# Optimization experiments

Measured on AMD Instinct MI355X. Metric: run time of the kernel, lower is better.

Reference implementation:

```python
import jax, jax.numpy as jnp
import numpy as np

B, F, L, D = 256, 4, 64, 768
HID = (F + F) * 200  # 1600
NEG = -1e10


def setup_inputs() -> dict:
    key = jax.random.key(0)
    ks = jax.random.split(key, 8)
    left = jax.random.normal(ks[0], (B, F, L, D), dtype=jnp.float32)
    right = jax.random.normal(ks[1], (B, F, L, D), dtype=jnp.float32)
    # emulate ragged padding: last quarter of tokens are zero (masked out)
    left = left.at[:, :, 3 * L // 4 :, :].set(0.0)
    right = right.at[:, :, 3 * L // 4 :, :].set(0.0)
    femb_l = jax.random.normal(ks[2], (F, D), dtype=jnp.float32)
    femb_r = jax.random.normal(ks[3], (F, D), dtype=jnp.float32)
    empty_attr = jax.random.normal(ks[4], (D,), dtype=jnp.float32) * 0.05
    in_dim = 2 * F * D
    W1 = jax.random.normal(ks[5], (HID, in_dim), dtype=jnp.float32) * (1.0 / np.sqrt(in_dim))
    b1 = jnp.zeros((HID,), dtype=jnp.float32)
    W2 = jax.random.normal(ks[6], (2, HID), dtype=jnp.float32) * (1.0 / np.sqrt(HID))
    b2 = jnp.full((2,), -np.log((1 - 0.01) / 0.01), dtype=jnp.float32)
    return {"left": left, "right": right, "femb_l": femb_l, "femb_r": femb_r,
            "empty_attr": empty_attr, "W1": W1, "b1": b1, "W2": W2, "b2": b2}


def _attribute_matching(v, femb, empty_attr):
    # v: [B, F, L, D], femb: [F, D]
    tok_mask = (v != 0).sum(axis=-1) > 0          # [B, F, L]
    attr_mask = tok_mask.any(axis=-1)              # [B, F]
    logits = jnp.einsum('bfld,fd->bfl', v, femb)   # per-field attention scores
    logits = logits + jnp.where(tok_mask, 0.0, NEG)
    w = jax.nn.softmax(logits, axis=2)             # masked softmax over tokens
    summary = jnp.einsum('bfl,bfld->bfd', w, v)    # attention pooling
    return jnp.where(attr_mask[..., None], summary, empty_attr)  # [B, F, D]


def reference(left, right, femb_l, femb_r, empty_attr, W1, b1, W2, b2):
    l_rep = _attribute_matching(left, femb_l, empty_attr)
    r_rep = _attribute_matching(right, femb_r, empty_attr)
    concat = jnp.concatenate([l_rep, r_rep], axis=1).reshape(left.shape[0], -1)
    h = jax.nn.relu(concat @ W1.T + b1)
    return h @ W2.T + b2  # [B, 2]
```

## Files before the change

### kernel.cpp

```cpp
#include <hip/hip_runtime.h>

typedef __attribute__((ext_vector_type(8))) short short8;
typedef __attribute__((ext_vector_type(4))) short short4_t;
typedef __attribute__((ext_vector_type(4))) float f32x4;

#define NEGBIG -1e10f

__device__ __forceinline__ unsigned short f2bf(float x) {
  unsigned int u = __float_as_uint(x);
  u += 0x7FFFu + ((u >> 16) & 1u);
  return (unsigned short)(u >> 16);
}
__device__ __forceinline__ unsigned pack2(float a, float b) {
  unsigned ua = __float_as_uint(a), ub = __float_as_uint(b);
  ua += 0x7FFFu + ((ua >> 16) & 1u);
  ub += 0x7FFFu + ((ub >> 16) & 1u);
  return (ua >> 16) | (ub & 0xFFFF0000u);
}
__device__ __forceinline__ float lo_bf(unsigned p) { return __uint_as_float(p << 16); }
__device__ __forceinline__ float hi_bf(unsigned p) { return __uint_as_float(p & 0xFFFF0000u); }

__device__ __forceinline__ float4 mul4(float4 a, float s) {
  float4 r; r.x = a.x*s; r.y = a.y*s; r.z = a.z*s; r.w = a.w*s; return r;
}
__device__ __forceinline__ float4 add4(float4 a, float4 b) {
  float4 r; r.x = a.x+b.x; r.y = a.y+b.y; r.z = a.z+b.z; r.w = a.w+b.w; return r;
}

__global__ __launch_bounds__(256) void pool_partial(
    const float* __restrict__ left, const float* __restrict__ right,
    const float* __restrict__ femb_l, const float* __restrict__ femb_r,
    float* __restrict__ partials,
    float4* __restrict__ meta)
{
  int bid   = blockIdx.x;
  int panel = bid >> 1;
  int half  = bid & 1;
  int side  = panel >> 10;
  int rem   = panel & 1023;
  int f     = rem & 3;
  const float* v    = (side ? right : left) + (size_t)rem * 64 * 768 + (size_t)half * 32 * 768;
  const float* femb = (side ? femb_r : femb_l) + f * 768;

  int tid = threadIdx.x, wave = tid >> 6, lane = tid & 63;

  const float4* fp = (const float4*)femb;
  float4 f0 = fp[lane], f1 = fp[lane + 64], f2 = fp[lane + 128];

  const float4* vp = (const float4*)(v + (size_t)wave * 8 * 768);

  float d[8];
  unsigned pk0[8], pk1[8], pk2[8], pk3[8], pk4[8], pk5[8];
  unsigned nzmask = 0;

  #pragma unroll
  for (int t = 0; t < 8; ++t) {
    float4 x0 = vp[t * 192 + lane];
    float4 x1 = vp[t * 192 + 64 + lane];
    float4 x2 = vp[t * 192 + 128 + lane];
    d[t] = x0.x*f0.x + x0.y*f0.y + x0.z*f0.z + x0.w*f0.w
         + x1.x*f1.x + x1.y*f1.y + x1.z*f1.z + x1.w*f1.w
         + x2.x*f2.x + x2.y*f2.y + x2.z*f2.z + x2.w*f2.w;
    unsigned nzb = __float_as_uint(x0.x) | __float_as_uint(x0.y)
                 | __float_as_uint(x0.z) | __float_as_uint(x0.w)
                 | __float_as_uint(x1.x) | __float_as_uint(x1.y)
                 | __float_as_uint(x1.z) | __float_as_uint(x1.w)
                 | __float_as_uint(x2.x) | __float_as_uint(x2.y)
                 | __float_as_uint(x2.z) | __float_as_uint(x2.w);
    nzmask |= (nzb != 0u) ? (1u << t) : 0u;
    pk0[t] = pack2(x0.x, x0.y); pk1[t] = pack2(x0.z, x0.w);
    pk2[t] = pack2(x1.x, x1.y); pk3[t] = pack2(x1.z, x1.w);
    pk4[t] = pack2(x2.x, x2.y); pk5[t] = pack2(x2.z, x2.w);
  }

  #pragma unroll
  for (int sh = 32; sh > 0; sh >>= 1) {
    d[0] += __shfl_xor(d[0], sh);
    d[1] += __shfl_xor(d[1], sh);
    d[2] += __shfl_xor(d[2], sh);
    d[3] += __shfl_xor(d[3], sh);
    d[4] += __shfl_xor(d[4], sh);
    d[5] += __shfl_xor(d[5], sh);
    d[6] += __shfl_xor(d[6], sh);
    d[7] += __shfl_xor(d[7], sh);
    nzmask |= __shfl_xor(nzmask, sh);
  }

  float l[8], e[8];
  #pragma unroll
  for (int t = 0; t < 8; ++t)
    l[t] = d[t] + (((nzmask >> t) & 1u) ? 0.f : NEGBIG);
  float m01 = fmaxf(l[0], l[1]), m23 = fmaxf(l[2], l[3]);
  float m45 = fmaxf(l[4], l[5]), m67 = fmaxf(l[6], l[7]);
  float m_w = fmaxf(fmaxf(m01, m23), fmaxf(m45, m67));
  #pragma unroll
  for (int t = 0; t < 8; ++t) e[t] = __expf(l[t] - m_w);
  float s_w = ((e[0]+e[1]) + (e[2]+e[3])) + ((e[4]+e[5]) + (e[6]+e[7]));

  __shared__ float m_lds[4], s_lds[4];
  __shared__ int   nz_lds[4];
  __shared__ float acc_lds[4 * 768];

  if (lane == 0) { m_lds[wave] = m_w; s_lds[wave] = s_w; nz_lds[wave] = (nzmask != 0u); }

  float4 A0 = {0,0,0,0}, A1 = {0,0,0,0}, A2 = {0,0,0,0};
  #pragma unroll
  for (int t = 0; t < 8; ++t) {
    float c = e[t];
    A0.x += c * lo_bf(pk0[t]); A0.y += c * hi_bf(pk0[t]);
    A0.z += c * lo_bf(pk1[t]); A0.w += c * hi_bf(pk1[t]);
    A1.x += c * lo_bf(pk2[t]); A1.y += c * hi_bf(pk2[t]);
    A1.z += c * lo_bf(pk3[t]); A1.w += c * hi_bf(pk3[t]);
    A2.x += c * lo_bf(pk4[t]); A2.y += c * hi_bf(pk4[t]);
    A2.z += c * lo_bf(pk5[t]); A2.w += c * hi_bf(pk5[t]);
  }

  __syncthreads();
  float M = fmaxf(fmaxf(m_lds[0], m_lds[1]), fmaxf(m_lds[2], m_lds[3]));
  float S = s_lds[0] * __expf(m_lds[0] - M) + s_lds[1] * __expf(m_lds[1] - M)
          + s_lds[2] * __expf(m_lds[2] - M) + s_lds[3] * __expf(m_lds[3] - M);
  float scale = __expf(m_w - M);

  float4* al = (float4*)acc_lds;
  al[wave * 192 +       lane] = mul4(A0, scale);
  al[wave * 192 +  64 + lane] = mul4(A1, scale);
  al[wave * 192 + 128 + lane] = mul4(A2, scale);
  __syncthreads();

  if (tid < 192) {
    float4 A = add4(add4(al[tid], al[192 + tid]),
                    add4(al[384 + tid], al[576 + tid]));
    ((float4*)(partials + (size_t)bid * 768))[tid] = A;
  }
  if (tid == 192) {
    int has = nz_lds[0] | nz_lds[1] | nz_lds[2] | nz_lds[3];
    float4 mt; mt.x = M; mt.y = S; mt.z = has ? 1.f : 0.f; mt.w = 0.f;
    meta[bid] = mt;
  }
}

__global__ __launch_bounds__(192) void pool_merge(
    const float* __restrict__ partials, const float4* __restrict__ meta,
    const float* __restrict__ empty_attr,
    unsigned short* __restrict__ concat)
{
  int panel = blockIdx.x;
  int tid = threadIdx.x;
  int side = panel >> 10;
  int rem  = panel & 1023;
  int f    = rem & 3;
  int b    = rem >> 2;

  float4 mt0 = meta[panel * 2], mt1 = meta[panel * 2 + 1];
  float M = fmaxf(mt0.x, mt1.x);
  float sc0 = __expf(mt0.x - M), sc1 = __expf(mt1.x - M);
  float S = mt0.y * sc0 + mt1.y * sc1;
  int has = (mt0.z != 0.f) | (mt1.z != 0.f);

  float4 A0 = ((const float4*)(partials + (size_t)(panel * 2) * 768))[tid];
  float4 A1 = ((const float4*)(partials + (size_t)(panel * 2 + 1) * 768))[tid];
  float4 r;
  if (has) {
    float inv = 1.f / S;
    r = add4(mul4(A0, sc0 * inv), mul4(A1, sc1 * inv));
  } else {
    r = ((const float4*)empty_attr)[tid];
  }
  ushort4 o;
  o.x = f2bf(r.x); o.y = f2bf(r.y); o.z = f2bf(r.z); o.w = f2bf(r.w);
  size_t base = ((size_t)b * 8 + side * 4 + f) * 192;
  ((ushort4*)concat)[base + tid] = o;
}

__global__ __launch_bounds__(256) void gemm1_kernel(
    const unsigned short* __restrict__ A,
    const float* __restrict__ W1,
    float* __restrict__ Hpart)
{
  const int K = 6144, N = 1600, KC = 768;
  int colb = blockIdx.x;
  int kc   = blockIdx.y;
  int col0 = colb * 16;
  int tid = threadIdx.x, wave = tid >> 6, lane = tid & 63;

  __shared__ short wlds[96 * 16 * 8];

  const float* wsrc = W1 + (size_t)col0 * K + kc * KC;
  #pragma unroll
  for (int i = 0; i < 12; ++i) {
    int flat4 = tid + 256 * i;
    int col = flat4 / 192;
    int k   = (flat4 % 192) * 4;
    float4 w = *(const float4*)(wsrc + (size_t)col * K + k);
    short4_t o;
    o[0] = (short)f2bf(w.x); o[1] = (short)f2bf(w.y);
    o[2] = (short)f2bf(w.z); o[3] = (short)f2bf(w.w);
    *(short4_t*)(wlds + (k >> 3) * 128 + col * 8 + (k & 7)) = o;
  }
  __syncthreads();

  int lr = lane & 15;
  const short* a0 = (const short*)A + (size_t)(wave * 64 + lr) * K + kc * KC + (lane >> 4) * 8;
  const short* bptr = wlds + (lane >> 4) * 128 + lr * 8;

  f32x4 acc0 = {}, acc1 = {}, acc2 = {}, acc3 = {};

  #pragma unroll 4
  for (int ks = 0; ks < 24; ++ks) {
    short8 bf  = *(const short8*)(bptr + ks * 512);
    short8 af0 = *(const short8*)(a0 + ks * 32);
    short8 af1 = *(const short8*)(a0 + ks * 32 + 16 * K);
    short8 af2 = *(const short8*)(a0 + ks * 32 + 32 * K);
    short8 af3 = *(const short8*)(a0 + ks * 32 + 48 * K);
    acc0 = __builtin_amdgcn_mfma_f32_16x16x32_bf16(af0, bf, acc0, 0, 0, 0);
    acc1 = __builtin_amdgcn_mfma_f32_16x16x32_bf16(af1, bf, acc1, 0, 0, 0);
    acc2 = __builtin_amdgcn_mfma_f32_16x16x32_bf16(af2, bf, acc2, 0, 0, 0);
    acc3 = __builtin_amdgcn_mfma_f32_16x16x32_bf16(af3, bf, acc3, 0, 0, 0);
  }

  int ccol = lane & 15;
  int crow = (lane >> 4) * 4;
  float* hp = Hpart + (size_t)kc * 256 * N + (size_t)col0 + ccol;
  f32x4 accs[4] = {acc0, acc1, acc2, acc3};
  #pragma unroll
  for (int i = 0; i < 4; ++i) {
    int r = wave * 64 + i * 16 + crow;
    #pragma unroll
    for (int q = 0; q < 4; ++q)
      hp[(size_t)(r + q) * N] = accs[i][q];
  }
}

__global__ __launch_bounds__(256) void epilogue_kernel(
    const float* __restrict__ Hpart, const float* __restrict__ b1,
    const float* __restrict__ W2, const float* __restrict__ b2,
    float* __restrict__ out)
{
  const int N = 1600;
  int b = blockIdx.x, tid = threadIdx.x;
  int wave = tid >> 6, lane = tid & 63;
  float s0 = 0.f, s1 = 0.f;
  for (int c = tid; c < N; c += 256) {
    float acc = 0.f;
    #pragma unroll
    for (int kc = 0; kc < 8; ++kc)
      acc += Hpart[((size_t)kc * 256 + b) * N + c];
    float h = fmaxf(acc + b1[c], 0.f);
    s0 += h * W2[c];
    s1 += h * W2[N + c];
  }
  #pragma unroll
  for (int s = 32; s > 0; s >>= 1) {
    s0 += __shfl_xor(s0, s);
    s1 += __shfl_xor(s1, s);
  }
  __shared__ float r0[4], r1[4];
  if (lane == 0) { r0[wave] = s0; r1[wave] = s1; }
  __syncthreads();
  if (tid == 0) {
    out[b * 2 + 0] = r0[0] + r0[1] + r0[2] + r0[3] + b2[0];
    out[b * 2 + 1] = r1[0] + r1[1] + r1[2] + r1[3] + b2[1];
  }
}

extern "C" void kernel_launch(void* const* d_in, const int* in_sizes, int n_in,
                              void* d_out, int out_size, void* d_ws, size_t ws_size,
                              hipStream_t stream) {
  const float* left       = (const float*)d_in[0];
  const float* right      = (const float*)d_in[1];
  const float* femb_l     = (const float*)d_in[2];
  const float* femb_r     = (const float*)d_in[3];
  const float* empty_attr = (const float*)d_in[4];
  const float* W1         = (const float*)d_in[5];
  const float* b1         = (const float*)d_in[6];
  const float* W2         = (const float*)d_in[7];
  const float* b2         = (const float*)d_in[8];
  float* out = (float*)d_out;

  char* ws = (char*)d_ws;
  unsigned short* concat = (unsigned short*)ws;
  float*          Hpart  = (float*)(ws + 3145728);
  float*  partials = Hpart;
  float4* meta     = (float4*)(ws + 3145728 + 12582912);

  hipLaunchKernelGGL(pool_partial, dim3(4096), dim3(256), 0, stream,
                     left, right, femb_l, femb_r, partials, meta);
  hipLaunchKernelGGL(pool_merge, dim3(2048), dim3(192), 0, stream,
                     partials, meta, empty_attr, concat);
  hipLaunchKernelGGL(gemm1_kernel, dim3(100, 8), dim3(256), 0, stream,
                     concat, W1, Hpart);
  hipLaunchKernelGGL(epilogue_kernel, dim3(256), dim3(256), 0, stream,
                     Hpart, b1, W2, b2, out);
}
```

Before: 139.6 us.

## Split pooling into quarter-panel blocks and store partials in bf16

Each pooling block now handles 16 tokens instead of 32, doubling the grid to 8192 blocks with fewer live registers per thread and an occupancy hint in launch bounds. Partial sums are written as bf16 instead of fp32, and the merge kernel combines four partials with log-sum-exp rescaling. This aims to improve memory latency hiding on the bandwidth-bound input read and to cut intermediate traffic. In exchange it adds one more rounding step on the partial sums, and the merge kernel does more work.

```diff
diff --git a/kernel.cpp b/kernel.cpp
--- a/kernel.cpp
+++ b/kernel.cpp
@@ -19,6 +19,7 @@
 }
 __device__ __forceinline__ float lo_bf(unsigned p) { return __uint_as_float(p << 16); }
 __device__ __forceinline__ float hi_bf(unsigned p) { return __uint_as_float(p & 0xFFFF0000u); }
+__device__ __forceinline__ float bfu(unsigned short h) { return __uint_as_float(((unsigned)h) << 16); }
 
 __device__ __forceinline__ float4 mul4(float4 a, float s) {
   float4 r; r.x = a.x*s; r.y = a.y*s; r.z = a.z*s; r.w = a.w*s; return r;
@@ -27,19 +28,19 @@
   float4 r; r.x = a.x+b.x; r.y = a.y+b.y; r.z = a.z+b.z; r.w = a.w+b.w; return r;
 }
 
-__global__ __launch_bounds__(256) void pool_partial(
+__global__ __launch_bounds__(256, 4) void pool_partial(
     const float* __restrict__ left, const float* __restrict__ right,
     const float* __restrict__ femb_l, const float* __restrict__ femb_r,
-    float* __restrict__ partials,
+    unsigned short* __restrict__ partials,
     float4* __restrict__ meta)
 {
-  int bid   = blockIdx.x;
-  int panel = bid >> 1;
-  int half  = bid & 1;
-  int side  = panel >> 10;
-  int rem   = panel & 1023;
-  int f     = rem & 3;
-  const float* v    = (side ? right : left) + (size_t)rem * 64 * 768 + (size_t)half * 32 * 768;
+  int bid     = blockIdx.x;
+  int panel   = bid >> 2;
+  int quarter = bid & 3;
+  int side    = panel >> 10;
+  int rem     = panel & 1023;
+  int f       = rem & 3;
+  const float* v    = (side ? right : left) + (size_t)rem * 64 * 768 + (size_t)quarter * 16 * 768;
   const float* femb = (side ? femb_r : femb_l) + f * 768;
 
   int tid = threadIdx.x, wave = tid >> 6, lane = tid & 63;
@@ -47,30 +48,47 @@
   const float4* fp = (const float4*)femb;
   float4 f0 = fp[lane], f1 = fp[lane + 64], f2 = fp[lane + 128];
 
-  const float4* vp = (const float4*)(v + (size_t)wave * 8 * 768);
-
-  float d[8];
-  unsigned pk0[8], pk1[8], pk2[8], pk3[8], pk4[8], pk5[8];
+  const float4* vp = (const float4*)(v + (size_t)wave * 4 * 768);
+
+  float d[4];
+  unsigned pk[4][6];
   unsigned nzmask = 0;
 
   #pragma unroll
-  for (int t = 0; t < 8; ++t) {
-    float4 x0 = vp[t * 192 + lane];
-    float4 x1 = vp[t * 192 + 64 + lane];
-    float4 x2 = vp[t * 192 + 128 + lane];
-    d[t] = x0.x*f0.x + x0.y*f0.y + x0.z*f0.z + x0.w*f0.w
-         + x1.x*f1.x + x1.y*f1.y + x1.z*f1.z + x1.w*f1.w
-         + x2.x*f2.x + x2.y*f2.y + x2.z*f2.z + x2.w*f2.w;
-    unsigned nzb = __float_as_uint(x0.x) | __float_as_uint(x0.y)
-                 | __float_as_uint(x0.z) | __float_as_uint(x0.w)
-                 | __float_as_uint(x1.x) | __float_as_uint(x1.y)
-                 | __float_as_uint(x1.z) | __float_as_uint(x1.w)
-                 | __float_as_uint(x2.x) | __float_as_uint(x2.y)
-                 | __float_as_uint(x2.z) | __float_as_uint(x2.w);
-    nzmask |= (nzb != 0u) ? (1u << t) : 0u;
-    pk0[t] = pack2(x0.x, x0.y); pk1[t] = pack2(x0.z, x0.w);
-    pk2[t] = pack2(x1.x, x1.y); pk3[t] = pack2(x1.z, x1.w);
-    pk4[t] = pack2(x2.x, x2.y); pk5[t] = pack2(x2.z, x2.w);
+  for (int g = 0; g < 2; ++g) {
+    const float4* ta = vp + (g * 2 + 0) * 192 + lane;
+    const float4* tb = vp + (g * 2 + 1) * 192 + lane;
+    float4 xa0 = ta[0], xa1 = ta[64], xa2 = ta[128];
+    float4 xb0 = tb[0], xb1 = tb[64], xb2 = tb[128];
+
+    int t0 = g * 2, t1 = g * 2 + 1;
+    d[t0] = xa0.x*f0.x + xa0.y*f0.y + xa0.z*f0.z + xa0.w*f0.w
+          + xa1.x*f1.x + xa1.y*f1.y + xa1.z*f1.z + xa1.w*f1.w
+          + xa2.x*f2.x + xa2.y*f2.y + xa2.z*f2.z + xa2.w*f2.w;
+    unsigned nza = __float_as_uint(xa0.x) | __float_as_uint(xa0.y)
+                 | __float_as_uint(xa0.z) | __float_as_uint(xa0.w)
+                 | __float_as_uint(xa1.x) | __float_as_uint(xa1.y)
+                 | __float_as_uint(xa1.z) | __float_as_uint(xa1.w)
+                 | __float_as_uint(xa2.x) | __float_as_uint(xa2.y)
+                 | __float_as_uint(xa2.z) | __float_as_uint(xa2.w);
+    nzmask |= (nza != 0u) ? (1u << t0) : 0u;
+    pk[t0][0] = pack2(xa0.x, xa0.y); pk[t0][1] = pack2(xa0.z, xa0.w);
+    pk[t0][2] = pack2(xa1.x, xa1.y); pk[t0][3] = pack2(xa1.z, xa1.w);
+    pk[t0][4] = pack2(xa2.x, xa2.y); pk[t0][5] = pack2(xa2.z, xa2.w);
+
+    d[t1] = xb0.x*f0.x + xb0.y*f0.y + xb0.z*f0.z + xb0.w*f0.w
+          + xb1.x*f1.x + xb1.y*f1.y + xb1.z*f1.z + xb1.w*f1.w
+          + xb2.x*f2.x + xb2.y*f2.y + xb2.z*f2.z + xb2.w*f2.w;
+    unsigned nzb = __float_as_uint(xb0.x) | __float_as_uint(xb0.y)
+                 | __float_as_uint(xb0.z) | __float_as_uint(xb0.w)
+                 | __float_as_uint(xb1.x) | __float_as_uint(xb1.y)
+                 | __float_as_uint(xb1.z) | __float_as_uint(xb1.w)
+                 | __float_as_uint(xb2.x) | __float_as_uint(xb2.y)
+                 | __float_as_uint(xb2.z) | __float_as_uint(xb2.w);
+    nzmask |= (nzb != 0u) ? (1u << t1) : 0u;
+    pk[t1][0] = pack2(xb0.x, xb0.y); pk[t1][1] = pack2(xb0.z, xb0.w);
+    pk[t1][2] = pack2(xb1.x, xb1.y); pk[t1][3] = pack2(xb1.z, xb1.w);
+    pk[t1][4] = pack2(xb2.x, xb2.y); pk[t1][5] = pack2(xb2.z, xb2.w);
   }
 
   #pragma unroll
@@ -79,23 +97,17 @@
     d[1] += __shfl_xor(d[1], sh);
     d[2] += __shfl_xor(d[2], sh);
     d[3] += __shfl_xor(d[3], sh);
-    d[4] += __shfl_xor(d[4], sh);
-    d[5] += __shfl_xor(d[5], sh);
-    d[6] += __shfl_xor(d[6], sh);
-    d[7] += __shfl_xor(d[7], sh);
     nzmask |= __shfl_xor(nzmask, sh);
   }
 
-  float l[8], e[8];
-  #pragma unroll
-  for (int t = 0; t < 8; ++t)
+  float l[4], e[4];
+  #pragma unroll
+  for (int t = 0; t < 4; ++t)
     l[t] = d[t] + (((nzmask >> t) & 1u) ? 0.f : NEGBIG);
-  float m01 = fmaxf(l[0], l[1]), m23 = fmaxf(l[2], l[3]);
-  float m45 = fmaxf(l[4], l[5]), m67 = fmaxf(l[6], l[7]);
-  float m_w = fmaxf(fmaxf(m01, m23), fmaxf(m45, m67));
-  #pragma unroll
-  for (int t = 0; t < 8; ++t) e[t] = __expf(l[t] - m_w);
-  float s_w = ((e[0]+e[1]) + (e[2]+e[3])) + ((e[4]+e[5]) + (e[6]+e[7]));
+  float m_w = fmaxf(fmaxf(l[0], l[1]), fmaxf(l[2], l[3]));
+  #pragma unroll
+  for (int t = 0; t < 4; ++t) e[t] = __expf(l[t] - m_w);
+  float s_w = (e[0] + e[1]) + (e[2] + e[3]);
 
   __shared__ float m_lds[4], s_lds[4];
   __shared__ int   nz_lds[4];
@@ -105,14 +117,14 @@
 
   float4 A0 = {0,0,0,0}, A1 = {0,0,0,0}, A2 = {0,0,0,0};
   #pragma unroll
-  for (int t = 0; t < 8; ++t) {
+  for (int t = 0; t < 4; ++t) {
     float c = e[t];
-    A0.x += c * lo_bf(pk0[t]); A0.y += c * hi_bf(pk0[t]);
-    A0.z += c * lo_bf(pk1[t]); A0.w += c * hi_bf(pk1[t]);
-    A1.x += c * lo_bf(pk2[t]); A1.y += c * hi_bf(pk2[t]);
-    A1.z += c * lo_bf(pk3[t]); A1.w += c * hi_bf(pk3[t]);
-    A2.x += c * lo_bf(pk4[t]); A2.y += c * hi_bf(pk4[t]);
-    A2.z += c * lo_bf(pk5[t]); A2.w += c * hi_bf(pk5[t]);
+    A0.x += c * lo_bf(pk[t][0]); A0.y += c * hi_bf(pk[t][0]);
+    A0.z += c * lo_bf(pk[t][1]); A0.w += c * hi_bf(pk[t][1]);
+    A1.x += c * lo_bf(pk[t][2]); A1.y += c * hi_bf(pk[t][2]);
+    A1.z += c * lo_bf(pk[t][3]); A1.w += c * hi_bf(pk[t][3]);
+    A2.x += c * lo_bf(pk[t][4]); A2.y += c * hi_bf(pk[t][4]);
+    A2.z += c * lo_bf(pk[t][5]); A2.w += c * hi_bf(pk[t][5]);
   }
 
   __syncthreads();
@@ -130,7 +142,9 @@
   if (tid < 192) {
     float4 A = add4(add4(al[tid], al[192 + tid]),
                     add4(al[384 + tid], al[576 + tid]));
-    ((float4*)(partials + (size_t)bid * 768))[tid] = A;
+    ushort4 o;
+    o.x = f2bf(A.x); o.y = f2bf(A.y); o.z = f2bf(A.z); o.w = f2bf(A.w);
+    ((ushort4*)(partials + (size_t)bid * 768))[tid] = o;
   }
   if (tid == 192) {
     int has = nz_lds[0] | nz_lds[1] | nz_lds[2] | nz_lds[3];
@@ -140,7 +154,7 @@
 }
 
 __global__ __launch_bounds__(192) void pool_merge(
-    const float* __restrict__ partials, const float4* __restrict__ meta,
+    const unsigned short* __restrict__ partials, const float4* __restrict__ meta,
     const float* __restrict__ empty_attr,
     unsigned short* __restrict__ concat)
 {
@@ -151,18 +165,26 @@
   int f    = rem & 3;
   int b    = rem >> 2;
 
-  float4 mt0 = meta[panel * 2], mt1 = meta[panel * 2 + 1];
-  float M = fmaxf(mt0.x, mt1.x);
+  int p4 = panel * 4;
+  float4 mt0 = meta[p4], mt1 = meta[p4 + 1], mt2 = meta[p4 + 2], mt3 = meta[p4 + 3];
+  float M = fmaxf(fmaxf(mt0.x, mt1.x), fmaxf(mt2.x, mt3.x));
   float sc0 = __expf(mt0.x - M), sc1 = __expf(mt1.x - M);
-  float S = mt0.y * sc0 + mt1.y * sc1;
-  int has = (mt0.z != 0.f) | (mt1.z != 0.f);
-
-  float4 A0 = ((const float4*)(partials + (size_t)(panel * 2) * 768))[tid];
-  float4 A1 = ((const float4*)(partials + (size_t)(panel * 2 + 1) * 768))[tid];
+  float sc2 = __expf(mt2.x - M), sc3 = __expf(mt3.x - M);
+  float S = mt0.y * sc0 + mt1.y * sc1 + mt2.y * sc2 + mt3.y * sc3;
+  int has = (mt0.z + mt1.z + mt2.z + mt3.z) != 0.f;
+
+  ushort4 q0 = ((const ushort4*)(partials + (size_t)(p4 + 0) * 768))[tid];
+  ushort4 q1 = ((const ushort4*)(partials + (size_t)(p4 + 1) * 768))[tid];
+  ushort4 q2 = ((const ushort4*)(partials + (size_t)(p4 + 2) * 768))[tid];
+  ushort4 q3 = ((const ushort4*)(partials + (size_t)(p4 + 3) * 768))[tid];
+
   float4 r;
   if (has) {
-    float inv = 1.f / S;
-    r = add4(mul4(A0, sc0 * inv), mul4(A1, sc1 * inv));
+    float i0 = sc0 / S, i1 = sc1 / S, i2 = sc2 / S, i3 = sc3 / S;
+    r.x = bfu(q0.x)*i0 + bfu(q1.x)*i1 + bfu(q2.x)*i2 + bfu(q3.x)*i3;
+    r.y = bfu(q0.y)*i0 + bfu(q1.y)*i1 + bfu(q2.y)*i2 + bfu(q3.y)*i3;
+    r.z = bfu(q0.z)*i0 + bfu(q1.z)*i1 + bfu(q2.z)*i2 + bfu(q3.z)*i3;
+    r.w = bfu(q0.w)*i0 + bfu(q1.w)*i1 + bfu(q2.w)*i2 + bfu(q3.w)*i3;
   } else {
     r = ((const float4*)empty_attr)[tid];
   }
@@ -280,10 +302,10 @@
   char* ws = (char*)d_ws;
   unsigned short* concat = (unsigned short*)ws;
   float*          Hpart  = (float*)(ws + 3145728);
-  float*  partials = Hpart;
-  float4* meta     = (float4*)(ws + 3145728 + 12582912);
-
-  hipLaunchKernelGGL(pool_partial, dim3(4096), dim3(256), 0, stream,
+  unsigned short* partials = (unsigned short*)Hpart;
+  float4*         meta     = (float4*)(ws + 3145728 + 12582912);
+
+  hipLaunchKernelGGL(pool_partial, dim3(8192), dim3(256), 0, stream,
                      left, right, femb_l, femb_r, partials, meta);
   hipLaunchKernelGGL(pool_merge, dim3(2048), dim3(192), 0, stream,
                      partials, meta, empty_attr, concat);
```

Result: no change. 139.6 us (+0.0%).

## Software-pipeline token loads with inline asm and store pooling partials as bf16

Applied to the files above, without the earlier changes.

Replaces the unrolled token-load loop in pool_partial with explicit inline-asm global_load_dwordx4 batches, double-buffered two tokens at a time, with manual s_waitcnt vmcnt so several loads stay in flight while earlier tokens are consumed. It also stores per-half pooled partials as bf16 instead of fp32, which halves the intermediate traffic between pool_partial and pool_merge, and moves the meta buffer offset to match. The costs are extra rounding of the partial sums before normalization and fragile hand-scheduled asm that relies on exact vmcnt accounting. The leading full vmcnt(0) wait on the femb loads also serializes the start of each wave.

```diff
diff --git a/kernel.cpp b/kernel.cpp
--- a/kernel.cpp
+++ b/kernel.cpp
@@ -19,6 +19,7 @@
 }
 __device__ __forceinline__ float lo_bf(unsigned p) { return __uint_as_float(p << 16); }
 __device__ __forceinline__ float hi_bf(unsigned p) { return __uint_as_float(p & 0xFFFF0000u); }
+__device__ __forceinline__ float bfu(unsigned short h) { return __uint_as_float(((unsigned)h) << 16); }
 
 __device__ __forceinline__ float4 mul4(float4 a, float s) {
   float4 r; r.x = a.x*s; r.y = a.y*s; r.z = a.z*s; r.w = a.w*s; return r;
@@ -30,7 +31,7 @@
 __global__ __launch_bounds__(256) void pool_partial(
     const float* __restrict__ left, const float* __restrict__ right,
     const float* __restrict__ femb_l, const float* __restrict__ femb_r,
-    float* __restrict__ partials,
+    unsigned short* __restrict__ partials,
     float4* __restrict__ meta)
 {
   int bid   = blockIdx.x;
@@ -47,31 +48,63 @@
   const float4* fp = (const float4*)femb;
   float4 f0 = fp[lane], f1 = fp[lane + 64], f2 = fp[lane + 128];
 
-  const float4* vp = (const float4*)(v + (size_t)wave * 8 * 768);
-
+  asm volatile("s_waitcnt vmcnt(0)" ::: "memory");
+  __builtin_amdgcn_sched_barrier(0);
+
+  const float* vw = v + (size_t)wave * 8 * 768;
+
+  float4 xa[6], xb[6];
   float d[8];
-  unsigned pk0[8], pk1[8], pk2[8], pk3[8], pk4[8], pk5[8];
+  unsigned pk[8][6];
   unsigned nzmask = 0;
 
-  #pragma unroll
-  for (int t = 0; t < 8; ++t) {
-    float4 x0 = vp[t * 192 + lane];
-    float4 x1 = vp[t * 192 + 64 + lane];
-    float4 x2 = vp[t * 192 + 128 + lane];
-    d[t] = x0.x*f0.x + x0.y*f0.y + x0.z*f0.z + x0.w*f0.w
-         + x1.x*f1.x + x1.y*f1.y + x1.z*f1.z + x1.w*f1.w
-         + x2.x*f2.x + x2.y*f2.y + x2.z*f2.z + x2.w*f2.w;
-    unsigned nzb = __float_as_uint(x0.x) | __float_as_uint(x0.y)
-                 | __float_as_uint(x0.z) | __float_as_uint(x0.w)
-                 | __float_as_uint(x1.x) | __float_as_uint(x1.y)
-                 | __float_as_uint(x1.z) | __float_as_uint(x1.w)
-                 | __float_as_uint(x2.x) | __float_as_uint(x2.y)
-                 | __float_as_uint(x2.z) | __float_as_uint(x2.w);
-    nzmask |= (nzb != 0u) ? (1u << t) : 0u;
-    pk0[t] = pack2(x0.x, x0.y); pk1[t] = pack2(x0.z, x0.w);
-    pk2[t] = pack2(x1.x, x1.y); pk3[t] = pack2(x1.z, x1.w);
-    pk4[t] = pack2(x2.x, x2.y); pk5[t] = pack2(x2.z, x2.w);
-  }
+  #define ISSUE_TOK(a0_, a1_, a2_, p_)                                        \
+    asm volatile("global_load_dwordx4 %0, %3, off\n\t"                        \
+                 "global_load_dwordx4 %1, %3, off offset:1024\n\t"            \
+                 "global_load_dwordx4 %2, %3, off offset:2048"                \
+                 : "=&v"(a0_), "=&v"(a1_), "=&v"(a2_) : "v"(p_))
+
+  #define ISSUE_BATCH(arr, tok0)                                              \
+    { const float* _pA = vw + (tok0) * 768 + lane * 4;                        \
+      const float* _pB = _pA + 768;                                           \
+      ISSUE_TOK(arr[0], arr[1], arr[2], _pA);                                 \
+      ISSUE_TOK(arr[3], arr[4], arr[5], _pB); }
+
+  #define WAITN(n)                                                            \
+    asm volatile("s_waitcnt vmcnt(" #n ")" ::: "memory");                     \
+    __builtin_amdgcn_sched_barrier(0);
+
+  #define CONSUME_TOK(t, y0, y1, y2)                                          \
+    { d[t] = y0.x*f0.x + y0.y*f0.y + y0.z*f0.z + y0.w*f0.w                    \
+           + y1.x*f1.x + y1.y*f1.y + y1.z*f1.z + y1.w*f1.w                    \
+           + y2.x*f2.x + y2.y*f2.y + y2.z*f2.z + y2.w*f2.w;                   \
+      unsigned nzb = __float_as_uint(y0.x) | __float_as_uint(y0.y)            \
+                   | __float_as_uint(y0.z) | __float_as_uint(y0.w)            \
+                   | __float_as_uint(y1.x) | __float_as_uint(y1.y)            \
+                   | __float_as_uint(y1.z) | __float_as_uint(y1.w)            \
+                   | __float_as_uint(y2.x) | __float_as_uint(y2.y)            \
+                   | __float_as_uint(y2.z) | __float_as_uint(y2.w);           \
+      nzmask |= (nzb != 0u) ? (1u << (t)) : 0u;                               \
+      pk[t][0] = pack2(y0.x, y0.y); pk[t][1] = pack2(y0.z, y0.w);             \
+      pk[t][2] = pack2(y1.x, y1.y); pk[t][3] = pack2(y1.z, y1.w);             \
+      pk[t][4] = pack2(y2.x, y2.y); pk[t][5] = pack2(y2.z, y2.w); }
+
+  ISSUE_BATCH(xa, 0);
+  ISSUE_BATCH(xb, 2);
+  WAITN(6);
+  CONSUME_TOK(0, xa[0], xa[1], xa[2]);
+  CONSUME_TOK(1, xa[3], xa[4], xa[5]);
+  ISSUE_BATCH(xa, 4);
+  WAITN(6);
+  CONSUME_TOK(2, xb[0], xb[1], xb[2]);
+  CONSUME_TOK(3, xb[3], xb[4], xb[5]);
+  ISSUE_BATCH(xb, 6);
+  WAITN(6);
+  CONSUME_TOK(4, xa[0], xa[1], xa[2]);
+  CONSUME_TOK(5, xa[3], xa[4], xa[5]);
+  WAITN(0);
+  CONSUME_TOK(6, xb[0], xb[1], xb[2]);
+  CONSUME_TOK(7, xb[3], xb[4], xb[5]);
 
   #pragma unroll
   for (int sh = 32; sh > 0; sh >>= 1) {
@@ -107,12 +140,12 @@
   #pragma unroll
   for (int t = 0; t < 8; ++t) {
     float c = e[t];
-    A0.x += c * lo_bf(pk0[t]); A0.y += c * hi_bf(pk0[t]);
-    A0.z += c * lo_bf(pk1[t]); A0.w += c * hi_bf(pk1[t]);
-    A1.x += c * lo_bf(pk2[t]); A1.y += c * hi_bf(pk2[t]);
-    A1.z += c * lo_bf(pk3[t]); A1.w += c * hi_bf(pk3[t]);
-    A2.x += c * lo_bf(pk4[t]); A2.y += c * hi_bf(pk4[t]);
-    A2.z += c * lo_bf(pk5[t]); A2.w += c * hi_bf(pk5[t]);
+    A0.x += c * lo_bf(pk[t][0]); A0.y += c * hi_bf(pk[t][0]);
+    A0.z += c * lo_bf(pk[t][1]); A0.w += c * hi_bf(pk[t][1]);
+    A1.x += c * lo_bf(pk[t][2]); A1.y += c * hi_bf(pk[t][2]);
+    A1.z += c * lo_bf(pk[t][3]); A1.w += c * hi_bf(pk[t][3]);
+    A2.x += c * lo_bf(pk[t][4]); A2.y += c * hi_bf(pk[t][4]);
+    A2.z += c * lo_bf(pk[t][5]); A2.w += c * hi_bf(pk[t][5]);
   }
 
   __syncthreads();
@@ -130,7 +163,9 @@
   if (tid < 192) {
     float4 A = add4(add4(al[tid], al[192 + tid]),
                     add4(al[384 + tid], al[576 + tid]));
-    ((float4*)(partials + (size_t)bid * 768))[tid] = A;
+    ushort4 o;
+    o.x = f2bf(A.x); o.y = f2bf(A.y); o.z = f2bf(A.z); o.w = f2bf(A.w);
+    ((ushort4*)(partials + (size_t)bid * 768))[tid] = o;
   }
   if (tid == 192) {
     int has = nz_lds[0] | nz_lds[1] | nz_lds[2] | nz_lds[3];
@@ -140,7 +175,7 @@
 }
 
 __global__ __launch_bounds__(192) void pool_merge(
-    const float* __restrict__ partials, const float4* __restrict__ meta,
+    const unsigned short* __restrict__ partials, const float4* __restrict__ meta,
     const float* __restrict__ empty_attr,
     unsigned short* __restrict__ concat)
 {
@@ -155,14 +190,18 @@
   float M = fmaxf(mt0.x, mt1.x);
   float sc0 = __expf(mt0.x - M), sc1 = __expf(mt1.x - M);
   float S = mt0.y * sc0 + mt1.y * sc1;
-  int has = (mt0.z != 0.f) | (mt1.z != 0.f);
-
-  float4 A0 = ((const float4*)(partials + (size_t)(panel * 2) * 768))[tid];
-  float4 A1 = ((const float4*)(partials + (size_t)(panel * 2 + 1) * 768))[tid];
+  int has = (mt0.z + mt1.z) != 0.f;
+
+  ushort4 q0 = ((const ushort4*)(partials + (size_t)(panel * 2 + 0) * 768))[tid];
+  ushort4 q1 = ((const ushort4*)(partials + (size_t)(panel * 2 + 1) * 768))[tid];
+
   float4 r;
   if (has) {
-    float inv = 1.f / S;
-    r = add4(mul4(A0, sc0 * inv), mul4(A1, sc1 * inv));
+    float i0 = sc0 / S, i1 = sc1 / S;
+    r.x = bfu(q0.x)*i0 + bfu(q1.x)*i1;
+    r.y = bfu(q0.y)*i0 + bfu(q1.y)*i1;
+    r.z = bfu(q0.z)*i0 + bfu(q1.z)*i1;
+    r.w = bfu(q0.w)*i0 + bfu(q1.w)*i1;
   } else {
     r = ((const float4*)empty_attr)[tid];
   }
@@ -280,8 +319,8 @@
   char* ws = (char*)d_ws;
   unsigned short* concat = (unsigned short*)ws;
   float*          Hpart  = (float*)(ws + 3145728);
-  float*  partials = Hpart;
-  float4* meta     = (float4*)(ws + 3145728 + 12582912);
+  unsigned short* partials = (unsigned short*)Hpart;
+  float4*         meta     = (float4*)(ws + 3145728 + 6291456);
 
   hipLaunchKernelGGL(pool_partial, dim3(4096), dim3(256), 0, stream,
                      left, right, femb_l, femb_r, partials, meta);
```

Result: no change. 138.8 us (-0.6%).
